# Optimization experiments

Measured on AMD Instinct MI355X. Metric: run time of the kernel, lower is better.

## Reference

```python
import jax, jax.numpy as jnp
import numpy as np

# static config
B, L, D = 2, 4096, 1024
H, G, WIN = 16, 2, 256
HD = D // H            # 64
KV = G * HD            # 128 (k/v proj width)
E, HID, TOPK = 8, 1024, 2
ENT_W, MAX_USE, EPS = 0.05, 0.4, 1e-8


def setup_inputs() -> dict:
    key = jax.random.key(0)
    ks = jax.random.split(key, 16)
    s = 0.02
    return {
        "x": jax.random.normal(ks[0], (B, L, D), jnp.float32),
        "Wq": jax.random.normal(ks[1], (D, D), jnp.float32) * s,
        "bq": jnp.zeros((D,), jnp.float32),
        "Wk": jax.random.normal(ks[2], (D, KV), jnp.float32) * s,
        "bk": jnp.zeros((KV,), jnp.float32),
        "Wv": jax.random.normal(ks[3], (D, KV), jnp.float32) * s,
        "bv": jnp.zeros((KV,), jnp.float32),
        "Wo": jax.random.normal(ks[4], (D, D), jnp.float32) * s,
        "bo": jnp.zeros((D,), jnp.float32),
        "ln1_g": jnp.ones((D,), jnp.float32),
        "ln1_b": jnp.zeros((D,), jnp.float32),
        "ln2_g": jnp.ones((D,), jnp.float32),
        "ln2_b": jnp.zeros((D,), jnp.float32),
        "Wg": jax.random.normal(ks[5], (D, E), jnp.float32) * 0.01,
        "bg": jnp.zeros((E,), jnp.float32),
        "We": jax.random.normal(ks[6], (E, D, HID), jnp.float32) * s,
        "be": jnp.zeros((E, HID), jnp.float32),
    }


def _layernorm(x, g, b):
    mu = jnp.mean(x, axis=-1, keepdims=True)
    var = jnp.var(x, axis=-1, keepdims=True)
    return (x - mu) * jax.lax.rsqrt(var + 1e-5) * g + b


def _local_attn(x, Wq, bq, Wk, bk, Wv, bv, Wo, bo):
    # overlapping sliding-window bidirectional GQA attention (dropout off / eval)
    Bx, Lx, _ = x.shape
    pad = (-Lx) % WIN
    xp = jnp.pad(x, ((0, 0), (0, pad), (0, 0)))
    Lp = Lx + pad
    q = (xp @ Wq + bq).reshape(Bx, Lp, H, HD).transpose(0, 2, 1, 3)   # [B,H,Lp,hd]
    k = (xp @ Wk + bk).reshape(Bx, Lp, G, HD).transpose(0, 2, 1, 3)   # [B,G,Lp,hd]
    v = (xp @ Wv + bv).reshape(Bx, Lp, G, HD).transpose(0, 2, 1, 3)
    stride = WIN // 2
    nw = (Lp - WIN) // stride + 1
    win_idx = (np.arange(nw)[:, None] * stride + np.arange(WIN)[None, :])
    qw = q[:, :, win_idx]
    kw = k[:, :, win_idx]
    vw = v[:, :, win_idx]
    rep = H // G
    # torch .repeat tiles kv groups: head h uses group h % G, i.e. h = r*G + g
    qw = qw.reshape(Bx, rep, G, nw, WIN, HD)
    scores = jnp.einsum('brgnqd,bgnkd->brgnqk', qw, kw) / np.sqrt(HD)
    attn = jax.nn.softmax(scores, axis=-1)
    o = jnp.einsum('brgnqk,bgnkd->brgnqd', attn, vw)
    o = o.reshape(Bx, H, nw, WIN, HD).transpose(0, 2, 3, 1, 4).reshape(Bx, nw * WIN, D)
    o = o[:, :Lx]                             # truncate concatenated windows to L
    return o @ Wo + bo


def _moe(x, Wg, bg, We, be):
    Bx, Lx, _ = x.shape
    xf = x.reshape(-1, D)                     # [N,D]
    N = xf.shape[0]
    probs = jax.nn.softmax(xf @ Wg + bg, axis=-1)          # [N,E]
    entropy = -jnp.sum(probs * jnp.log(probs + EPS), axis=-1).mean()
    ent_loss = ENT_W * entropy
    topk_p, topk_i = jax.lax.top_k(probs, TOPK)            # [N,K]
    # dense grouped-GEMM reference for top-k dispatch/combine
    all_out = jnp.einsum('nd,edh->neh', xf, We) + be       # [N,E,HID]
    wts = jnp.zeros((N, E), xf.dtype).at[jnp.arange(N)[:, None], topk_i].add(topk_p)
    out = jnp.einsum('ne,neh->nh', wts, all_out)           # [N,HID]
    counts = jnp.zeros((E,), xf.dtype).at[topk_i.reshape(-1)].add(1.0)
    usage = counts / (N + EPS)
    penalty = jnp.sum(jax.nn.relu(usage - MAX_USE))
    return out.reshape(Bx, Lx, HID), ent_loss + penalty


def reference(x, Wq, bq, Wk, bk, Wv, bv, Wo, bo, ln1_g, ln1_b, ln2_g, ln2_b, Wg, bg, We, be):
    h = x + _local_attn(_layernorm(x, ln1_g, ln1_b), Wq, bq, Wk, bk, Wv, bv, Wo, bo)
    moe_out, aux = _moe(_layernorm(h, ln2_g, ln2_b), Wg, bg, We, be)
    out = h + moe_out
    return out, aux
```

## Files before the change

### kernel.cpp

```cpp
#include <hip/hip_runtime.h>
#include <hip/hip_bf16.h>
#include <stdint.h>

typedef __attribute__((ext_vector_type(8))) short bf16x8;
typedef __attribute__((ext_vector_type(8))) _Float16 f16x8;
typedef __attribute__((ext_vector_type(4))) _Float16 f16x4;
typedef __attribute__((ext_vector_type(4))) float f32x4;

__device__ __forceinline__ short f2bf(float f) {
  __hip_bfloat16 h = __float2bfloat16(f);
  union { __hip_bfloat16 h; short s; } u; u.h = h; return u.s;
}

__device__ __forceinline__ unsigned pk2(float a, float b) {
  union { _Float16 h; unsigned short s; } ua, ub;
  ua.h = (_Float16)a; ub.h = (_Float16)b;
  return (unsigned)ua.s | ((unsigned)ub.s << 16);
}

__device__ __forceinline__ void gld16(const void* g, void* l) {
  __builtin_amdgcn_global_load_lds((const __attribute__((address_space(1))) void*)g,
                                   (__attribute__((address_space(3))) void*)l, 16, 0, 0);
}

__device__ __forceinline__ float wave_sum64(float v) {
  #pragma unroll
  for (int off = 1; off < 64; off <<= 1) v += __shfl_xor(v, off);
  return v;
}
__device__ __forceinline__ double wave_sum64d(double v) {
  #pragma unroll
  for (int off = 1; off < 64; off <<= 1) v += __shfl_xor(v, off);
  return v;
}

__global__ __launch_bounds__(256) void ln_split(const float* __restrict__ x,
    const float* __restrict__ g, const float* __restrict__ b,
    _Float16* __restrict__ xh, _Float16* __restrict__ xl) {
  int t = blockIdx.x, tid = threadIdx.x;
  const float4 v = ((const float4*)(x + (size_t)t * 1024))[tid];
  float s = v.x + v.y + v.z + v.w;
  float s2 = v.x*v.x + v.y*v.y + v.z*v.z + v.w*v.w;
  s = wave_sum64(s); s2 = wave_sum64(s2);
  __shared__ float pa[4], pb[4];
  int wid = tid >> 6, lane = tid & 63;
  if (lane == 0) { pa[wid] = s; pb[wid] = s2; }
  __syncthreads();
  float S = pa[0]+pa[1]+pa[2]+pa[3], S2 = pb[0]+pb[1]+pb[2]+pb[3];
  float mu = S * (1.f/1024.f);
  float var = S2 * (1.f/1024.f) - mu*mu;
  float rs = rsqrtf(var + 1e-5f);
  const float4 gv = ((const float4*)g)[tid];
  const float4 bv = ((const float4*)b)[tid];
  float4 o;
  o.x = (v.x-mu)*rs*gv.x + bv.x; o.y = (v.y-mu)*rs*gv.y + bv.y;
  o.z = (v.z-mu)*rs*gv.z + bv.z; o.w = (v.w-mu)*rs*gv.w + bv.w;
  f16x4 hv, lv;
  hv.x = (_Float16)o.x; lv.x = (_Float16)((o.x - (float)hv.x)*2048.f);
  hv.y = (_Float16)o.y; lv.y = (_Float16)((o.y - (float)hv.y)*2048.f);
  hv.z = (_Float16)o.z; lv.z = (_Float16)((o.z - (float)hv.z)*2048.f);
  hv.w = (_Float16)o.w; lv.w = (_Float16)((o.w - (float)hv.w)*2048.f);
  *(f16x4*)&xh[(size_t)t*1024 + tid*4] = hv;
  *(f16x4*)&xl[(size_t)t*1024 + tid*4] = lv;
}

__global__ __launch_bounds__(256) void ln_bf16(const float* __restrict__ x,
    const float* __restrict__ g, const float* __restrict__ b, short* __restrict__ out,
    float2* __restrict__ murs) {
  int t = blockIdx.x, tid = threadIdx.x;
  const float4 v = ((const float4*)(x + (size_t)t * 1024))[tid];
  float s = v.x + v.y + v.z + v.w;
  float s2 = v.x*v.x + v.y*v.y + v.z*v.z + v.w*v.w;
  s = wave_sum64(s); s2 = wave_sum64(s2);
  __shared__ float pa[4], pb[4];
  int wid = tid >> 6, lane = tid & 63;
  if (lane == 0) { pa[wid] = s; pb[wid] = s2; }
  __syncthreads();
  float S = pa[0]+pa[1]+pa[2]+pa[3], S2 = pb[0]+pb[1]+pb[2]+pb[3];
  float mu = S * (1.f/1024.f);
  float var = S2 * (1.f/1024.f) - mu*mu;
  float rs = rsqrtf(var + 1e-5f);
  if (tid == 0) murs[t] = make_float2(mu, rs);
  const float4 gv = ((const float4*)g)[tid];
  const float4 bv = ((const float4*)b)[tid];
  short4 o;
  o.x = f2bf((v.x-mu)*rs*gv.x + bv.x); o.y = f2bf((v.y-mu)*rs*gv.y + bv.y);
  o.z = f2bf((v.z-mu)*rs*gv.z + bv.z); o.w = f2bf((v.w-mu)*rs*gv.w + bv.w);
  ((short4*)(out + (size_t)t * 1024))[tid] = o;
}

__global__ void t_w_f16(const float* __restrict__ src, int srcN,
                        _Float16* __restrict__ dh, _Float16* __restrict__ dl, int dstRow0) {
  __shared__ float tile[32][33];
  int kt = blockIdx.x, nt = blockIdx.y;
  int tx = threadIdx.x, ty = threadIdx.y;
  #pragma unroll
  for (int i = 0; i < 4; i++)
    tile[ty + 8*i][tx] = src[(size_t)(kt*32 + ty + 8*i)*srcN + nt*32 + tx];
  __syncthreads();
  #pragma unroll
  for (int i = 0; i < 4; i++) {
    float v = tile[tx][ty + 8*i];
    _Float16 h = (_Float16)v;
    _Float16 l = (_Float16)((v - (float)h) * 2048.0f);
    size_t o = (size_t)(dstRow0 + nt*32 + ty + 8*i)*1024 + kt*32 + tx;
    dh[o] = h; dl[o] = l;
  }
}

template<int MODE>
__global__ __launch_bounds__(256, 3) void gemm_dma(
    const _Float16* __restrict__ Agh, const _Float16* __restrict__ Agl,
    const _Float16* __restrict__ BTh, const _Float16* __restrict__ BTl,
    const float* __restrict__ b0, const float* __restrict__ b1, const float* __restrict__ b2,
    const float* __restrict__ resid,
    float* __restrict__ out0, float* __restrict__ out1, float* __restrict__ out2) {
  int m0 = blockIdx.x * 64;
  int y = blockIdx.y;
  int n0 = y * 128;
  float* dst; const float* biasp; int dcol0, ld;
  if (MODE == 0) {
    if (y < 8)      { dst = out0; biasp = b0 + y*128; dcol0 = y*128; ld = 1024; }
    else if (y == 8){ dst = out1; biasp = b1; dcol0 = 0; ld = 128; }
    else            { dst = out2; biasp = b2; dcol0 = 0; ld = 128; }
  } else            { dst = out0; biasp = b0 + y*128; dcol0 = y*128; ld = 1024; }

  __shared__ _Float16 AhS[2][2048];
  __shared__ _Float16 AlS[2][2048];
  __shared__ _Float16 BhS[2][4096];
  __shared__ _Float16 BlS[2][4096];
  int tid = threadIdx.x;
  int lane = tid & 63, w = tid >> 6;
  int wm = (w & 1) * 32, wn = (w >> 1) * 64;
  int l15 = lane & 15, quad = lane >> 4;

  int Pa = tid;
  int cA = (Pa & 3) ^ ((Pa >> 3) & 3);
  size_t gA = (size_t)(m0 + (Pa >> 2)) * 1024 + cA * 8;
  int Pb0 = tid, Pb1 = tid + 256;
  int cB0 = (Pb0 & 3) ^ ((Pb0 >> 3) & 3);
  int cB1 = (Pb1 & 3) ^ ((Pb1 >> 3) & 3);
  size_t gB0 = (size_t)(n0 + (Pb0 >> 2)) * 1024 + cB0 * 8;
  size_t gB1 = (size_t)(n0 + (Pb1 >> 2)) * 1024 + cB1 * 8;

  f32x4 accM[2][4] = {};
  f32x4 accC[2][4] = {};

  gld16(Agh + gA, &AhS[0][Pa*8]);
  gld16(Agl + gA, &AlS[0][Pa*8]);
  gld16(BTh + gB0, &BhS[0][Pb0*8]);
  gld16(BTh + gB1, &BhS[0][Pb1*8]);
  gld16(BTl + gB0, &BlS[0][Pb0*8]);
  gld16(BTl + gB1, &BlS[0][Pb1*8]);
  __syncthreads();

  int cur = 0;
  for (int it = 0; it < 32; ++it) {
    if (it < 31) {
      int kb = (it + 1) * 32;
      int nb = cur ^ 1;
      gld16(Agh + gA + kb, &AhS[nb][Pa*8]);
      gld16(Agl + gA + kb, &AlS[nb][Pa*8]);
      gld16(BTh + gB0 + kb, &BhS[nb][Pb0*8]);
      gld16(BTh + gB1 + kb, &BhS[nb][Pb1*8]);
      gld16(BTl + gB0 + kb, &BlS[nb][Pb0*8]);
      gld16(BTl + gB1 + kb, &BlS[nb][Pb1*8]);
    }
    f16x8 bh[4], bl[4];
    #pragma unroll
    for (int nt = 0; nt < 4; nt++) {
      int row = wn + nt*16 + l15;
      int pc = quad ^ ((row >> 1) & 3);
      bh[nt] = *(const f16x8*)&BhS[cur][row*32 + pc*8];
      bl[nt] = *(const f16x8*)&BlS[cur][row*32 + pc*8];
    }
    #pragma unroll
    for (int mt = 0; mt < 2; mt++) {
      int row = wm + mt*16 + l15;
      int pc = quad ^ ((row >> 1) & 3);
      f16x8 ah = *(const f16x8*)&AhS[cur][row*32 + pc*8];
      f16x8 al = *(const f16x8*)&AlS[cur][row*32 + pc*8];
      #pragma unroll
      for (int nt = 0; nt < 4; nt++) {
        accM[mt][nt] = __builtin_amdgcn_mfma_f32_16x16x32_f16(ah, bh[nt], accM[mt][nt], 0, 0, 0);
        accC[mt][nt] = __builtin_amdgcn_mfma_f32_16x16x32_f16(ah, bl[nt], accC[mt][nt], 0, 0, 0);
        accC[mt][nt] = __builtin_amdgcn_mfma_f32_16x16x32_f16(al, bh[nt], accC[mt][nt], 0, 0, 0);
      }
    }
    __syncthreads();
    cur ^= 1;
  }

  const float inv2048 = 1.0f / 2048.0f;
  #pragma unroll
  for (int mt = 0; mt < 2; mt++)
    #pragma unroll
    for (int r = 0; r < 4; r++) {
      int row = m0 + wm + mt*16 + quad*4 + r;
      #pragma unroll
      for (int nt = 0; nt < 4; nt++) {
        int c = wn + nt*16 + l15;
        float v = accM[mt][nt][r] + accC[mt][nt][r]*inv2048 + biasp[c];
        if (MODE == 1) v += resid[(size_t)row*1024 + dcol0 + c];
        dst[(size_t)row*ld + dcol0 + c] = v;
      }
    }
}

__global__ __launch_bounds__(256, 2) void attn_mfma(
    const float* __restrict__ Qs, const float* __restrict__ Kf, const float* __restrict__ Vf,
    _Float16* __restrict__ Oh, _Float16* __restrict__ Ol) {
  int qb = blockIdx.x, n = blockIdx.y;
  int b = blockIdx.z >> 4, h = blockIdx.z & 15;
  int g = h & 1;
  int tid = threadIdx.x;
  int lane = tid & 63, w = tid >> 6;
  int l15 = lane & 15, quad = lane >> 4;

  __shared__ __align__(16) char smem[70912];
  _Float16* Vt = (_Float16*)smem;
  _Float16* Qh = (_Float16*)(smem + 33792);
  _Float16* Ql = (_Float16*)(smem + 43008);
  _Float16* Kh = (_Float16*)(smem + 52224);
  _Float16* Kl = (_Float16*)(smem + 61440);
  _Float16* Pm = (_Float16*)(smem + 33792);
  float*   linv = (float*)(smem + 70656);

  int qtok0 = b*4096 + n*128 + qb*64;
  int key0  = b*4096 + n*128;

  #pragma unroll
  for (int i = 0; i < 4; i++) {
    int idx = tid + 256*i;
    int row = idx >> 4, c4 = idx & 15;
    float4 v = *(const float4*)&Qs[(size_t)(qtok0+row)*1024 + h*64 + c4*4];
    f16x4 hv, lv;
    hv.x = (_Float16)v.x; lv.x = (_Float16)(v.x - (float)hv.x);
    hv.y = (_Float16)v.y; lv.y = (_Float16)(v.y - (float)hv.y);
    hv.z = (_Float16)v.z; lv.z = (_Float16)(v.z - (float)hv.z);
    hv.w = (_Float16)v.w; lv.w = (_Float16)(v.w - (float)hv.w);
    *(f16x4*)&Qh[row*72 + c4*4] = hv;
    *(f16x4*)&Ql[row*72 + c4*4] = lv;
  }
  {
    int kk = tid >> 4, dd = tid & 15;
    #pragma unroll
    for (int i = 0; i < 8; i++) {
      int p = i*16 + kk;
      float4 v0 = *(const float4*)&Vf[(size_t)(key0 + 2*p    )*128 + g*64 + dd*4];
      float4 v1 = *(const float4*)&Vf[(size_t)(key0 + 2*p + 1)*128 + g*64 + dd*4];
      *(unsigned*)&Vt[(dd*4+0)*264 + 2*p] = pk2(v0.x, v1.x);
      *(unsigned*)&Vt[(dd*4+1)*264 + 2*p] = pk2(v0.y, v1.y);
      *(unsigned*)&Vt[(dd*4+2)*264 + 2*p] = pk2(v0.z, v1.z);
      *(unsigned*)&Vt[(dd*4+3)*264 + 2*p] = pk2(v0.w, v1.w);
    }
  }
  __syncthreads();

  f16x8 qh[2], ql[2];
  {
    int qrow = (w*16 + l15)*72;
    qh[0] = *(const f16x8*)&Qh[qrow + quad*8];
    qh[1] = *(const f16x8*)&Qh[qrow + 32 + quad*8];
    ql[0] = *(const f16x8*)&Ql[qrow + quad*8];
    ql[1] = *(const f16x8*)&Ql[qrow + 32 + quad*8];
  }

  f32x4 S[16];
  #pragma unroll
  for (int t = 0; t < 16; t++) S[t] = (f32x4){0.f,0.f,0.f,0.f};

  for (int c = 0; c < 4; c++) {
    if (c) __syncthreads();
    #pragma unroll
    for (int i = 0; i < 4; i++) {
      int idx = tid + 256*i;
      int row = idx >> 4, c4 = idx & 15;
      float4 v = *(const float4*)&Kf[(size_t)(key0 + c*64 + row)*128 + g*64 + c4*4];
      f16x4 hv, lv;
      hv.x = (_Float16)v.x; lv.x = (_Float16)(v.x - (float)hv.x);
      hv.y = (_Float16)v.y; lv.y = (_Float16)(v.y - (float)hv.y);
      hv.z = (_Float16)v.z; lv.z = (_Float16)(v.z - (float)hv.z);
      hv.w = (_Float16)v.w; lv.w = (_Float16)(v.w - (float)hv.w);
      *(f16x4*)&Kh[row*72 + c4*4] = hv;
      *(f16x4*)&Kl[row*72 + c4*4] = lv;
    }
    __syncthreads();
    #pragma unroll
    for (int t = 0; t < 4; t++) {
      int krow = (t*16 + l15)*72;
      f16x8 kh0 = *(const f16x8*)&Kh[krow + quad*8];
      f16x8 kh1 = *(const f16x8*)&Kh[krow + 32 + quad*8];
      f16x8 kl0 = *(const f16x8*)&Kl[krow + quad*8];
      f16x8 kl1 = *(const f16x8*)&Kl[krow + 32 + quad*8];
      int ti = c*4 + t;
      S[ti] = __builtin_amdgcn_mfma_f32_16x16x32_f16(qh[0], kh0, S[ti], 0, 0, 0);
      S[ti] = __builtin_amdgcn_mfma_f32_16x16x32_f16(ql[0], kh0, S[ti], 0, 0, 0);
      S[ti] = __builtin_amdgcn_mfma_f32_16x16x32_f16(qh[0], kl0, S[ti], 0, 0, 0);
      S[ti] = __builtin_amdgcn_mfma_f32_16x16x32_f16(qh[1], kh1, S[ti], 0, 0, 0);
      S[ti] = __builtin_amdgcn_mfma_f32_16x16x32_f16(ql[1], kh1, S[ti], 0, 0, 0);
      S[ti] = __builtin_amdgcn_mfma_f32_16x16x32_f16(qh[1], kl1, S[ti], 0, 0, 0);
    }
  }

  float lrow[4];
  #pragma unroll
  for (int r = 0; r < 4; r++) {
    float mx = S[0][r];
    #pragma unroll
    for (int t = 1; t < 16; t++) mx = fmaxf(mx, S[t][r]);
    mx = fmaxf(mx, __shfl_xor(mx, 1)); mx = fmaxf(mx, __shfl_xor(mx, 2));
    mx = fmaxf(mx, __shfl_xor(mx, 4)); mx = fmaxf(mx, __shfl_xor(mx, 8));
    float sum = 0.f;
    #pragma unroll
    for (int t = 0; t < 16; t++) {
      float e = __expf((S[t][r] - mx) * 0.125f);
      S[t][r] = e; sum += e;
    }
    sum += __shfl_xor(sum, 1); sum += __shfl_xor(sum, 2);
    sum += __shfl_xor(sum, 4); sum += __shfl_xor(sum, 8);
    lrow[r] = sum;
  }
  if (l15 == 0) {
    #pragma unroll
    for (int r = 0; r < 4; r++) linv[w*16 + quad*4 + r] = 1.f / lrow[r];
  }
  __syncthreads();

  #pragma unroll
  for (int r = 0; r < 4; r++) {
    int q = w*16 + quad*4 + r;
    bool mine = (l15 & 1) ? (r >= 2) : (r < 2);
    #pragma unroll
    for (int t = 0; t < 16; t++) {
      float own = S[t][r];
      float oth = __shfl_xor(own, 1);
      if (mine) {
        float e0 = (l15 & 1) ? oth : own;
        float e1 = (l15 & 1) ? own : oth;
        *(unsigned*)&Pm[q*264 + t*16 + (l15 & ~1)] = pk2(e0, e1);
      }
    }
  }
  __syncthreads();

  f32x4 O[4];
  #pragma unroll
  for (int t = 0; t < 4; t++) O[t] = (f32x4){0.f,0.f,0.f,0.f};
  {
    int prow = (w*16 + l15)*264;
    #pragma unroll
    for (int ks = 0; ks < 8; ks++) {
      f16x8 pa = *(const f16x8*)&Pm[prow + ks*32 + quad*8];
      #pragma unroll
      for (int t = 0; t < 4; t++) {
        f16x8 vb = *(const f16x8*)&Vt[(t*16 + l15)*264 + ks*32 + quad*8];
        O[t] = __builtin_amdgcn_mfma_f32_16x16x32_f16(pa, vb, O[t], 0, 0, 0);
      }
    }
  }

  #pragma unroll
  for (int r = 0; r < 4; r++) {
    int qlocal = w*16 + quad*4 + r;
    float inv = linv[qlocal];
    int orow = b*4096 + n*256 + qb*64 + qlocal;
    #pragma unroll
    for (int t = 0; t < 4; t++) {
      float o = O[t][r] * inv;
      _Float16 oh = (_Float16)o;
      _Float16 ol = (_Float16)((o - (float)oh) * 2048.f);
      size_t oo = (size_t)orow*1024 + h*64 + t*16 + l15;
      Oh[oo] = oh; Ol[oo] = ol;
    }
  }
}

__global__ __launch_bounds__(256) void gating_logits(
    const float* __restrict__ h, const float2* __restrict__ murs,
    const float* __restrict__ g2, const float* __restrict__ b2,
    const float* __restrict__ Wg, const float* __restrict__ bg,
    int* __restrict__ e1e2, float2* __restrict__ p12, float* __restrict__ entArr) {
  int tid = threadIdx.x, lane = tid & 63, wid = tid >> 6;
  int tok = blockIdx.x*4 + wid;
  const float* row = h + (size_t)tok * 1024;
  float2 mr = murs[tok];
  double mu = (double)mr.x, rs = (double)mr.y;
  double acc[8] = {};
  #pragma unroll
  for (int q = 0; q < 4; q++) {
    float4 xv = ((const float4*)row)[lane*4 + q];
    float4 gv = ((const float4*)g2)[lane*4 + q];
    float4 bv = ((const float4*)b2)[lane*4 + q];
    float xs[4] = {xv.x, xv.y, xv.z, xv.w};
    float gs[4] = {gv.x, gv.y, gv.z, gv.w};
    float bs[4] = {bv.x, bv.y, bv.z, bv.w};
    #pragma unroll
    for (int j = 0; j < 4; j++) {
      int i = lane*16 + q*4 + j;
      double xn = ((double)xs[j] - mu) * rs * (double)gs[j] + (double)bs[j];
      const float4 w0 = *(const float4*)&Wg[(size_t)i*8];
      const float4 w1 = *(const float4*)&Wg[(size_t)i*8 + 4];
      acc[0] += xn*(double)w0.x; acc[1] += xn*(double)w0.y;
      acc[2] += xn*(double)w0.z; acc[3] += xn*(double)w0.w;
      acc[4] += xn*(double)w1.x; acc[5] += xn*(double)w1.y;
      acc[6] += xn*(double)w1.z; acc[7] += xn*(double)w1.w;
    }
  }
  #pragma unroll
  for (int e = 0; e < 8; e++) acc[e] = wave_sum64d(acc[e]) + (double)bg[e];
  int e1 = 0;
  #pragma unroll
  for (int e = 1; e < 8; e++) if (acc[e] > acc[e1]) e1 = e;
  int e2 = (e1 == 0) ? 1 : 0;
  #pragma unroll
  for (int e = 0; e < 8; e++) if (e != e1 && acc[e] > acc[e2]) e2 = e;
  float lf[8];
  #pragma unroll
  for (int e = 0; e < 8; e++) lf[e] = (float)acc[e];
  float mx = lf[0];
  #pragma unroll
  for (int e = 1; e < 8; e++) mx = fmaxf(mx, lf[e]);
  float ex[8], Z = 0.f;
  #pragma unroll
  for (int e = 0; e < 8; e++) { ex[e] = __expf(lf[e] - mx); Z += ex[e]; }
  float invZ = 1.f / Z, ent = 0.f;
  float p[8];
  #pragma unroll
  for (int e = 0; e < 8; e++) { p[e] = ex[e]*invZ; ent -= p[e]*__logf(p[e] + 1e-8f); }
  if (lane == 0) {
    e1e2[tok] = e1 | (e2 << 8);
    p12[tok]  = make_float2(p[e1], p[e2]);
    entArr[tok] = ent;
  }
}

__global__ __launch_bounds__(128) void scatter_kernel(
    const int* __restrict__ e1e2, const float2* __restrict__ p12,
    int* __restrict__ cnt, int* __restrict__ bucket, float* __restrict__ bucketP,
    int* __restrict__ bucketS) {
  __shared__ int lcnt[8], base[8];
  int tid = threadIdx.x;
  if (tid < 8) lcnt[tid] = 0;
  __syncthreads();
  int tok = blockIdx.x*128 + tid;
  int ee = e1e2[tok];
  int e1 = ee & 255, e2 = ee >> 8;
  float2 p = p12[tok];
  int o1 = atomicAdd(&lcnt[e1], 1);
  int o2 = atomicAdd(&lcnt[e2], 1);
  __syncthreads();
  if (tid < 8) base[tid] = atomicAdd(&cnt[tid], lcnt[tid]);
  __syncthreads();
  int i1 = base[e1] + o1;
  bucket[e1*8192 + i1] = tok; bucketP[e1*8192 + i1] = p.x; bucketS[e1*8192 + i1] = 0;
  int i2 = base[e2] + o2;
  bucket[e2*8192 + i2] = tok; bucketP[e2*8192 + i2] = p.y; bucketS[e2*8192 + i2] = 1;
}

__global__ __launch_bounds__(256) void aux_kernel(const float* __restrict__ entArr,
    const int* __restrict__ cnt, float* __restrict__ auxOut) {
  int tid = threadIdx.x;
  float s = 0.f;
  for (int i = tid; i < 8192; i += 256) s += entArr[i];
  s = wave_sum64(s);
  __shared__ float pa[4];
  if ((tid & 63) == 0) pa[tid >> 6] = s;
  __syncthreads();
  if (tid == 0) {
    float tot = pa[0]+pa[1]+pa[2]+pa[3];
    float entMean = tot / 8192.f;
    float pen = 0.f;
    for (int e = 0; e < 8; e++) {
      float usage = (float)cnt[e] / (8192.f + 1e-8f);
      pen += fmaxf(usage - 0.4f, 0.f);
    }
    auxOut[0] = 0.05f * entMean + pen;
  }
}

__global__ void transpose_We(const float* __restrict__ We, short* __restrict__ WeT) {
  int e = blockIdx.z;
  __shared__ float tile[32][33];
  int kt = blockIdx.x, nt = blockIdx.y;
  int tx = threadIdx.x, ty = threadIdx.y;
  const float* src = We + (size_t)e * 1048576;
  short* dst = WeT + (size_t)e * 1048576;
  #pragma unroll
  for (int i = 0; i < 4; i++)
    tile[ty + 8*i][tx] = src[(size_t)(kt*32 + ty + 8*i)*1024 + nt*32 + tx];
  __syncthreads();
  #pragma unroll
  for (int i = 0; i < 4; i++)
    dst[(size_t)(nt*32 + ty + 8*i)*1024 + kt*32 + tx] = f2bf(tile[tx][ty + 8*i]);
}

__global__ __launch_bounds__(256, 4) void moe_gemm(
    const short* __restrict__ hln, const short* __restrict__ WeT,
    const float* __restrict__ be, const int* __restrict__ cnt,
    const int* __restrict__ bucket, const float* __restrict__ bucketP,
    const int* __restrict__ bucketS,
    float* __restrict__ slot0, float* __restrict__ slot1) {
  int e = blockIdx.z;
  int count = cnt[e];
  int mtile = blockIdx.x;
  if (mtile * 128 >= count) return;
  int n0 = blockIdx.y * 128;
  __shared__ short As[2][4096];
  __shared__ short Bs[2][4096];
  __shared__ int   toks[128];
  __shared__ float pws[128];
  __shared__ int   sls[128];
  int tid = threadIdx.x;
  if (tid < 128) {
    int idx = mtile*128 + tid;
    int ic = idx < count ? idx : count - 1;
    toks[tid] = bucket[e*8192 + ic];
    pws[tid]  = bucketP[e*8192 + ic];
    sls[tid]  = bucketS[e*8192 + ic];
  }
  __syncthreads();
  int lane = tid & 63, w = tid >> 6;
  int wm = (w & 1) * 64, wn = (w >> 1) * 64;
  int l15 = lane & 15, quad = lane >> 4;
  const short* Bt = WeT + (size_t)e * 1048576;

  int P0 = tid, P1 = tid + 256;
  int c0 = (P0 & 3) ^ ((P0 >> 3) & 3);
  int c1 = (P1 & 3) ^ ((P1 >> 3) & 3);
  size_t gA0 = (size_t)toks[P0 >> 2] * 1024 + c0 * 8;
  size_t gA1 = (size_t)toks[P1 >> 2] * 1024 + c1 * 8;
  size_t gB0 = (size_t)(n0 + (P0 >> 2)) * 1024 + c0 * 8;
  size_t gB1 = (size_t)(n0 + (P1 >> 2)) * 1024 + c1 * 8;

  f32x4 acc[4][4] = {};

  gld16(hln + gA0, &As[0][P0*8]);
  gld16(hln + gA1, &As[0][P1*8]);
  gld16(Bt  + gB0, &Bs[0][P0*8]);
  gld16(Bt  + gB1, &Bs[0][P1*8]);
  __syncthreads();

  int cur = 0;
  for (int it = 0; it < 32; ++it) {
    if (it < 31) {
      int kb = (it + 1) * 32;
      int nb = cur ^ 1;
      gld16(hln + gA0 + kb, &As[nb][P0*8]);
      gld16(hln + gA1 + kb, &As[nb][P1*8]);
      gld16(Bt  + gB0 + kb, &Bs[nb][P0*8]);
      gld16(Bt  + gB1 + kb, &Bs[nb][P1*8]);
    }
    bf16x8 af[4], bfr[4];
    #pragma unroll
    for (int nt = 0; nt < 4; nt++) {
      int row = wn + nt*16 + l15;
      int pc = quad ^ ((row >> 1) & 3);
      bfr[nt] = *(const bf16x8*)&Bs[cur][row*32 + pc*8];
    }
    #pragma unroll
    for (int mt = 0; mt < 4; mt++) {
      int row = wm + mt*16 + l15;
      int pc = quad ^ ((row >> 1) & 3);
      af[mt] = *(const bf16x8*)&As[cur][row*32 + pc*8];
      #pragma unroll
      for (int nt = 0; nt < 4; nt++)
        acc[mt][nt] = __builtin_amdgcn_mfma_f32_16x16x32_bf16(af[mt], bfr[nt], acc[mt][nt], 0, 0, 0);
    }
    __syncthreads();
    cur ^= 1;
  }

  #pragma unroll
  for (int mt = 0; mt < 4; mt++) {
    #pragma unroll
    for (int r = 0; r < 4; r++) {
      int m = wm + mt*16 + quad*4 + r;
      if (mtile*128 + m < count) {
        int tok = toks[m];
        float pp = pws[m];
        float* dst = sls[m] ? slot1 : slot0;
        #pragma unroll
        for (int nt = 0; nt < 4; nt++) {
          int col = n0 + wn + nt*16 + l15;
          dst[(size_t)tok*1024 + col] = pp * (acc[mt][nt][r] + be[e*1024 + col]);
        }
      }
    }
  }
}

__global__ __launch_bounds__(256) void final_add(float* __restrict__ out,
    const float* __restrict__ s0, const float* __restrict__ s1) {
  const int total = 8388608 / 4;
  for (int i = blockIdx.x*256 + threadIdx.x; i < total; i += gridDim.x*256) {
    float4 a = ((float4*)out)[i];
    const float4 x0 = ((const float4*)s0)[i];
    const float4 x1 = ((const float4*)s1)[i];
    a.x += x0.x + x1.x; a.y += x0.y + x1.y; a.z += x0.z + x1.z; a.w += x0.w + x1.w;
    ((float4*)out)[i] = a;
  }
}

extern "C" void kernel_launch(void* const* d_in, const int* in_sizes, int n_in,
                              void* d_out, int out_size, void* d_ws, size_t ws_size,
                              hipStream_t stream) {
  const float* x    = (const float*)d_in[0];
  const float* Wq   = (const float*)d_in[1];
  const float* bq   = (const float*)d_in[2];
  const float* Wk   = (const float*)d_in[3];
  const float* bk   = (const float*)d_in[4];
  const float* Wv   = (const float*)d_in[5];
  const float* bv   = (const float*)d_in[6];
  const float* Wo   = (const float*)d_in[7];
  const float* bo   = (const float*)d_in[8];
  const float* ln1g = (const float*)d_in[9];
  const float* ln1b = (const float*)d_in[10];
  const float* ln2g = (const float*)d_in[11];
  const float* ln2b = (const float*)d_in[12];
  const float* Wg   = (const float*)d_in[13];
  const float* bg   = (const float*)d_in[14];
  const float* We   = (const float*)d_in[15];
  const float* be   = (const float*)d_in[16];
  float* out = (float*)d_out;

  char* ws = (char*)d_ws;
  size_t off = 0;
  auto alloc = [&](size_t bytes) { char* p = ws + off; off += (bytes + 255) & ~(size_t)255; return p; };
  _Float16* xh  = (_Float16*)alloc(16777216);
  _Float16* xl  = (_Float16*)alloc(16777216);
  float* Qs    = (float*)alloc(33554432);
  float* Kf    = (float*)alloc(4194304);
  float* Vf    = (float*)alloc(4194304);
  short* WeT   = (short*)alloc(16777216);
  float* slot0 = (float*)alloc(33554432);
  float* slot1 = (float*)alloc(33554432);
  int*   bucket  = (int*)alloc(262144);
  float* bucketP = (float*)alloc(262144);
  int*   bucketS = (int*)alloc(262144);
  int*   cnt     = (int*)alloc(256);
  float* entArr  = (float*)alloc(32768);
  int*   e1e2    = (int*)alloc(32768);
  float2* p12    = (float2*)alloc(65536);
  float2* murs   = (float2*)alloc(65536);
  _Float16* Oh = xh;
  _Float16* Ol = xl;
  short* hln   = (short*)Qs;
  _Float16* WoTh    = (_Float16*)slot0;
  _Float16* WoTl    = (_Float16*)(slot0 + 524288);
  _Float16* BTqkv_h = (_Float16*)slot1;
  _Float16* BTqkv_l = (_Float16*)((char*)slot1 + 2621440);

  hipMemsetAsync(cnt, 0, 256, stream);
  t_w_f16<<<dim3(32, 32), dim3(32, 8), 0, stream>>>(Wq, 1024, BTqkv_h, BTqkv_l, 0);
  t_w_f16<<<dim3(32, 4),  dim3(32, 8), 0, stream>>>(Wk, 128,  BTqkv_h, BTqkv_l, 1024);
  t_w_f16<<<dim3(32, 4),  dim3(32, 8), 0, stream>>>(Wv, 128,  BTqkv_h, BTqkv_l, 1152);
  t_w_f16<<<dim3(32, 32), dim3(32, 8), 0, stream>>>(Wo, 1024, WoTh, WoTl, 0);
  transpose_We<<<dim3(32,32,8), dim3(32,8), 0, stream>>>(We, WeT);

  ln_split<<<8192, 256, 0, stream>>>(x, ln1g, ln1b, xh, xl);
  gemm_dma<0><<<dim3(128,10), 256, 0, stream>>>(xh, xl, BTqkv_h, BTqkv_l, bq, bk, bv,
                                                nullptr, Qs, Kf, Vf);
  attn_mfma<<<dim3(4,16,32), 256, 0, stream>>>(Qs, Kf, Vf, Oh, Ol);
  gemm_dma<1><<<dim3(128,8), 256, 0, stream>>>(Oh, Ol, WoTh, WoTl, bo, nullptr, nullptr,
                                               x, out, nullptr, nullptr);
  ln_bf16<<<8192, 256, 0, stream>>>(out, ln2g, ln2b, hln, murs);
  gating_logits<<<2048, 256, 0, stream>>>(out, murs, ln2g, ln2b, Wg, bg, e1e2, p12, entArr);
  scatter_kernel<<<64, 128, 0, stream>>>(e1e2, p12, cnt, bucket, bucketP, bucketS);
  aux_kernel<<<1, 256, 0, stream>>>(entArr, cnt, out + 8388608);
  moe_gemm<<<dim3(64,8,8), 256, 0, stream>>>(hln, WeT, be, cnt, bucket, bucketP, bucketS, slot0, slot1);
  final_add<<<2048, 256, 0, stream>>>(out, slot0, slot1);
}
```

Baseline: 552.7 us.

## Fuse LN2 into gating kernel and make MoE GEMM grid-strided over M tiles

```diff
diff --git a/kernel.cpp b/kernel.cpp
--- a/kernel.cpp
+++ b/kernel.cpp
@@ -64,31 +64,6 @@
   *(f16x4*)&xl[(size_t)t*1024 + tid*4] = lv;
 }
 
-__global__ __launch_bounds__(256) void ln_bf16(const float* __restrict__ x,
-    const float* __restrict__ g, const float* __restrict__ b, short* __restrict__ out,
-    float2* __restrict__ murs) {
-  int t = blockIdx.x, tid = threadIdx.x;
-  const float4 v = ((const float4*)(x + (size_t)t * 1024))[tid];
-  float s = v.x + v.y + v.z + v.w;
-  float s2 = v.x*v.x + v.y*v.y + v.z*v.z + v.w*v.w;
-  s = wave_sum64(s); s2 = wave_sum64(s2);
-  __shared__ float pa[4], pb[4];
-  int wid = tid >> 6, lane = tid & 63;
-  if (lane == 0) { pa[wid] = s; pb[wid] = s2; }
-  __syncthreads();
-  float S = pa[0]+pa[1]+pa[2]+pa[3], S2 = pb[0]+pb[1]+pb[2]+pb[3];
-  float mu = S * (1.f/1024.f);
-  float var = S2 * (1.f/1024.f) - mu*mu;
-  float rs = rsqrtf(var + 1e-5f);
-  if (tid == 0) murs[t] = make_float2(mu, rs);
-  const float4 gv = ((const float4*)g)[tid];
-  const float4 bv = ((const float4*)b)[tid];
-  short4 o;
-  o.x = f2bf((v.x-mu)*rs*gv.x + bv.x); o.y = f2bf((v.y-mu)*rs*gv.y + bv.y);
-  o.z = f2bf((v.z-mu)*rs*gv.z + bv.z); o.w = f2bf((v.w-mu)*rs*gv.w + bv.w);
-  ((short4*)(out + (size_t)t * 1024))[tid] = o;
-}
-
 __global__ void t_w_f16(const float* __restrict__ src, int srcN,
                         _Float16* __restrict__ dh, _Float16* __restrict__ dl, int dstRow0) {
   __shared__ float tile[32][33];
@@ -376,29 +351,45 @@
   }
 }
 
-__global__ __launch_bounds__(256) void gating_logits(
-    const float* __restrict__ h, const float2* __restrict__ murs,
+__global__ __launch_bounds__(256) void ln2_gating(
+    const float* __restrict__ h,
     const float* __restrict__ g2, const float* __restrict__ b2,
     const float* __restrict__ Wg, const float* __restrict__ bg,
+    short* __restrict__ hln,
     int* __restrict__ e1e2, float2* __restrict__ p12, float* __restrict__ entArr) {
   int tid = threadIdx.x, lane = tid & 63, wid = tid >> 6;
   int tok = blockIdx.x*4 + wid;
   const float* row = h + (size_t)tok * 1024;
-  float2 mr = murs[tok];
-  double mu = (double)mr.x, rs = (double)mr.y;
-  double acc[8] = {};
+  float4 xv4[4];
+  float s = 0.f, s2 = 0.f;
   #pragma unroll
   for (int q = 0; q < 4; q++) {
     float4 xv = ((const float4*)row)[lane*4 + q];
+    xv4[q] = xv;
+    s  += xv.x + xv.y + xv.z + xv.w;
+    s2 += xv.x*xv.x + xv.y*xv.y + xv.z*xv.z + xv.w*xv.w;
+  }
+  s = wave_sum64(s); s2 = wave_sum64(s2);
+  float mu = s * (1.f/1024.f);
+  float var = s2 * (1.f/1024.f) - mu*mu;
+  float rs = rsqrtf(var + 1e-5f);
+  double mud = (double)mu, rsd = (double)rs;
+  double acc[8] = {};
+  short* hrow = hln + (size_t)tok * 1024;
+  #pragma unroll
+  for (int q = 0; q < 4; q++) {
+    float4 xv = xv4[q];
     float4 gv = ((const float4*)g2)[lane*4 + q];
     float4 bv = ((const float4*)b2)[lane*4 + q];
     float xs[4] = {xv.x, xv.y, xv.z, xv.w};
     float gs[4] = {gv.x, gv.y, gv.z, gv.w};
     float bs[4] = {bv.x, bv.y, bv.z, bv.w};
+    short os[4];
     #pragma unroll
     for (int j = 0; j < 4; j++) {
       int i = lane*16 + q*4 + j;
-      double xn = ((double)xs[j] - mu) * rs * (double)gs[j] + (double)bs[j];
+      os[j] = f2bf((xs[j] - mu) * rs * gs[j] + bs[j]);
+      double xn = ((double)xs[j] - mud) * rsd * (double)gs[j] + (double)bs[j];
       const float4 w0 = *(const float4*)&Wg[(size_t)i*8];
       const float4 w1 = *(const float4*)&Wg[(size_t)i*8 + 4];
       acc[0] += xn*(double)w0.x; acc[1] += xn*(double)w0.y;
@@ -406,6 +397,8 @@
       acc[4] += xn*(double)w1.x; acc[5] += xn*(double)w1.y;
       acc[6] += xn*(double)w1.z; acc[7] += xn*(double)w1.w;
     }
+    short4 o = make_short4(os[0], os[1], os[2], os[3]);
+    ((short4*)hrow)[lane*4 + q] = o;
   }
   #pragma unroll
   for (int e = 0; e < 8; e++) acc[e] = wave_sum64d(acc[e]) + (double)bg[e];
@@ -503,8 +496,6 @@
     float* __restrict__ slot0, float* __restrict__ slot1) {
   int e = blockIdx.z;
   int count = cnt[e];
-  int mtile = blockIdx.x;
-  if (mtile * 128 >= count) return;
   int n0 = blockIdx.y * 128;
   __shared__ short As[2][4096];
   __shared__ short Bs[2][4096];
@@ -512,14 +503,6 @@
   __shared__ float pws[128];
   __shared__ int   sls[128];
   int tid = threadIdx.x;
-  if (tid < 128) {
-    int idx = mtile*128 + tid;
-    int ic = idx < count ? idx : count - 1;
-    toks[tid] = bucket[e*8192 + ic];
-    pws[tid]  = bucketP[e*8192 + ic];
-    sls[tid]  = bucketS[e*8192 + ic];
-  }
-  __syncthreads();
   int lane = tid & 63, w = tid >> 6;
   int wm = (w & 1) * 64, wn = (w >> 1) * 64;
   int l15 = lane & 15, quad = lane >> 4;
@@ -528,62 +511,75 @@
   int P0 = tid, P1 = tid + 256;
   int c0 = (P0 & 3) ^ ((P0 >> 3) & 3);
   int c1 = (P1 & 3) ^ ((P1 >> 3) & 3);
-  size_t gA0 = (size_t)toks[P0 >> 2] * 1024 + c0 * 8;
-  size_t gA1 = (size_t)toks[P1 >> 2] * 1024 + c1 * 8;
   size_t gB0 = (size_t)(n0 + (P0 >> 2)) * 1024 + c0 * 8;
   size_t gB1 = (size_t)(n0 + (P1 >> 2)) * 1024 + c1 * 8;
 
-  f32x4 acc[4][4] = {};
-
-  gld16(hln + gA0, &As[0][P0*8]);
-  gld16(hln + gA1, &As[0][P1*8]);
-  gld16(Bt  + gB0, &Bs[0][P0*8]);
-  gld16(Bt  + gB1, &Bs[0][P1*8]);
-  __syncthreads();
-
-  int cur = 0;
-  for (int it = 0; it < 32; ++it) {
-    if (it < 31) {
-      int kb = (it + 1) * 32;
-      int nb = cur ^ 1;
-      gld16(hln + gA0 + kb, &As[nb][P0*8]);
-      gld16(hln + gA1 + kb, &As[nb][P1*8]);
-      gld16(Bt  + gB0 + kb, &Bs[nb][P0*8]);
-      gld16(Bt  + gB1 + kb, &Bs[nb][P1*8]);
-    }
-    bf16x8 af[4], bfr[4];
-    #pragma unroll
-    for (int nt = 0; nt < 4; nt++) {
-      int row = wn + nt*16 + l15;
-      int pc = quad ^ ((row >> 1) & 3);
-      bfr[nt] = *(const bf16x8*)&Bs[cur][row*32 + pc*8];
-    }
+  for (int mtile = blockIdx.x; mtile * 128 < count; mtile += 16) {
+    __syncthreads();
+    if (tid < 128) {
+      int idx = mtile*128 + tid;
+      int ic = idx < count ? idx : count - 1;
+      toks[tid] = bucket[e*8192 + ic];
+      pws[tid]  = bucketP[e*8192 + ic];
+      sls[tid]  = bucketS[e*8192 + ic];
+    }
+    __syncthreads();
+
+    size_t gA0 = (size_t)toks[P0 >> 2] * 1024 + c0 * 8;
+    size_t gA1 = (size_t)toks[P1 >> 2] * 1024 + c1 * 8;
+
+    f32x4 acc[4][4] = {};
+
+    gld16(hln + gA0, &As[0][P0*8]);
+    gld16(hln + gA1, &As[0][P1*8]);
+    gld16(Bt  + gB0, &Bs[0][P0*8]);
+    gld16(Bt  + gB1, &Bs[0][P1*8]);
+    __syncthreads();
+
+    int cur = 0;
+    for (int it = 0; it < 32; ++it) {
+      if (it < 31) {
+        int kb = (it + 1) * 32;
+        int nb = cur ^ 1;
+        gld16(hln + gA0 + kb, &As[nb][P0*8]);
+        gld16(hln + gA1 + kb, &As[nb][P1*8]);
+        gld16(Bt  + gB0 + kb, &Bs[nb][P0*8]);
+        gld16(Bt  + gB1 + kb, &Bs[nb][P1*8]);
+      }
+      bf16x8 af[4], bfr[4];
+      #pragma unroll
+      for (int nt = 0; nt < 4; nt++) {
+        int row = wn + nt*16 + l15;
+        int pc = quad ^ ((row >> 1) & 3);
+        bfr[nt] = *(const bf16x8*)&Bs[cur][row*32 + pc*8];
+      }
+      #pragma unroll
+      for (int mt = 0; mt < 4; mt++) {
+        int row = wm + mt*16 + l15;
+        int pc = quad ^ ((row >> 1) & 3);
+        af[mt] = *(const bf16x8*)&As[cur][row*32 + pc*8];
+        #pragma unroll
+        for (int nt = 0; nt < 4; nt++)
+          acc[mt][nt] = __builtin_amdgcn_mfma_f32_16x16x32_bf16(af[mt], bfr[nt], acc[mt][nt], 0, 0, 0);
+      }
+      __syncthreads();
+      cur ^= 1;
+    }
+
     #pragma unroll
     for (int mt = 0; mt < 4; mt++) {
-      int row = wm + mt*16 + l15;
-      int pc = quad ^ ((row >> 1) & 3);
-      af[mt] = *(const bf16x8*)&As[cur][row*32 + pc*8];
       #pragma unroll
-      for (int nt = 0; nt < 4; nt++)
-        acc[mt][nt] = __builtin_amdgcn_mfma_f32_16x16x32_bf16(af[mt], bfr[nt], acc[mt][nt], 0, 0, 0);
-    }
-    __syncthreads();
-    cur ^= 1;
-  }
-
-  #pragma unroll
-  for (int mt = 0; mt < 4; mt++) {
-    #pragma unroll
-    for (int r = 0; r < 4; r++) {
-      int m = wm + mt*16 + quad*4 + r;
-      if (mtile*128 + m < count) {
-        int tok = toks[m];
-        float pp = pws[m];
-        float* dst = sls[m] ? slot1 : slot0;
-        #pragma unroll
-        for (int nt = 0; nt < 4; nt++) {
-          int col = n0 + wn + nt*16 + l15;
-          dst[(size_t)tok*1024 + col] = pp * (acc[mt][nt][r] + be[e*1024 + col]);
+      for (int r = 0; r < 4; r++) {
+        int m = wm + mt*16 + quad*4 + r;
+        if (mtile*128 + m < count) {
+          int tok = toks[m];
+          float pp = pws[m];
+          float* dst = sls[m] ? slot1 : slot0;
+          #pragma unroll
+          for (int nt = 0; nt < 4; nt++) {
+            int col = n0 + wn + nt*16 + l15;
+            dst[(size_t)tok*1024 + col] = pp * (acc[mt][nt][r] + be[e*1024 + col]);
+          }
         }
       }
     }
@@ -642,7 +638,6 @@
   float* entArr  = (float*)alloc(32768);
   int*   e1e2    = (int*)alloc(32768);
   float2* p12    = (float2*)alloc(65536);
-  float2* murs   = (float2*)alloc(65536);
   _Float16* Oh = xh;
   _Float16* Ol = xl;
   short* hln   = (short*)Qs;
@@ -664,10 +659,9 @@
   attn_mfma<<<dim3(4,16,32), 256, 0, stream>>>(Qs, Kf, Vf, Oh, Ol);
   gemm_dma<1><<<dim3(128,8), 256, 0, stream>>>(Oh, Ol, WoTh, WoTl, bo, nullptr, nullptr,
                                                x, out, nullptr, nullptr);
-  ln_bf16<<<8192, 256, 0, stream>>>(out, ln2g, ln2b, hln, murs);
-  gating_logits<<<2048, 256, 0, stream>>>(out, murs, ln2g, ln2b, Wg, bg, e1e2, p12, entArr);
+  ln2_gating<<<2048, 256, 0, stream>>>(out, ln2g, ln2b, Wg, bg, hln, e1e2, p12, entArr);
   scatter_kernel<<<64, 128, 0, stream>>>(e1e2, p12, cnt, bucket, bucketP, bucketS);
   aux_kernel<<<1, 256, 0, stream>>>(entArr, cnt, out + 8388608);
-  moe_gemm<<<dim3(64,8,8), 256, 0, stream>>>(hln, WeT, be, cnt, bucket, bucketP, bucketS, slot0, slot1);
+  moe_gemm<<<dim3(16,8,8), 256, 0, stream>>>(hln, WeT, be, cnt, bucket, bucketP, bucketS, slot0, slot1);
   final_add<<<2048, 256, 0, stream>>>(out, slot0, slot1);
 }
```

New measurement: 532.7 us. 3.6% less time.
